# Kernel tuning notes

Measured on AMD Instinct MI355X. Metric: run time of the kernel, lower is better.

## Reference

```python
import jax, jax.numpy as jnp
import numpy as np


def _quat_to_rotT(q):
    # q: [..., 4] in (w, x, y, z) order, exactly mirroring the torch entry order,
    # including the final transpose(3, 2). Returns [..., 3, 3].
    w, x, y, z = q[..., 0], q[..., 1], q[..., 2], q[..., 3]
    R = jnp.stack([
        1.0 - 2.0 * (y ** 2 + z ** 2), 2.0 * x * y - 2.0 * w * z, 2.0 * w * y + 2.0 * x * z,
        2.0 * x * y + 2.0 * z * w, 1.0 - 2.0 * (x ** 2 + z ** 2), -2.0 * w * x + 2.0 * y * z,
        -2.0 * w * y + 2.0 * x * z, 2.0 * w * x + 2.0 * y * z, 1.0 - 2.0 * (x ** 2 + y ** 2),
    ], axis=-1).reshape(q.shape[:-1] + (3, 3))
    return jnp.swapaxes(R, -1, -2)


def _forward(pred_t, pred_r, pred_c, target_r, target_t, model_points, choose, symmetric, diameters, rot_anchors):
    bs, num_rot, _ = pred_r.shape
    # --- anchor regularization: cos_dist = bmm(pred_r, rot_anchors^T) ---
    cos_dist = jnp.einsum('brq,aq->bra', pred_r, rot_anchors)  # [bs, R, R]
    diag = jnp.diagonal(cos_dist, axis1=1, axis2=2)             # [bs, R]
    reg = jnp.max(cos_dist, axis=2) - diag
    loss_reg = jnp.mean(jnp.where(reg > 0.001, reg, 0.0))       # F.threshold(x, 0.001, 0)

    # --- rotate model points by every anchor-refined rotation ---
    rotT = _quat_to_rotT(pred_r)                                 # [bs, R, 3, 3]
    mp = model_points[:, 0]                                      # [bs, N, 3]
    pred_pts = jnp.einsum('bnk,brkj->brnj', mp, rotT)            # [bs, R, N, 3]
    tgt = target_r[:, 0]                                         # [bs, M, 3]

    # symmetric branch: pairwise distances via the |a|^2+|b|^2-2ab expansion
    # (avoids materializing the [bs,R,N,M,3] difference tensor; dist tensor only)
    a2 = jnp.sum(pred_pts ** 2, axis=-1)                         # [bs, R, N]
    b2 = jnp.sum(tgt ** 2, axis=-1)                              # [bs, M]
    ab = jnp.einsum('brnk,bmk->brnm', pred_pts, tgt)             # [bs, R, N, M]
    d2 = a2[:, :, :, None] + b2[:, None, None, :] - 2.0 * ab
    dist_pair = jnp.sqrt(jnp.maximum(d2, 1e-12))
    sym_d = jnp.mean(jnp.min(dist_pair, axis=3), axis=2)         # [bs, R]

    # non-symmetric branch: pointwise distance (M == N)
    nonsym_d = jnp.mean(
        jnp.linalg.norm(pred_pts - tgt[:, None, :, :], axis=-1), axis=2)  # [bs, R]

    d = jnp.where(symmetric[:, None], sym_d, nonsym_d)           # [bs, R]
    per_anchor = d / (diameters[:, None] * pred_c) + jnp.log(pred_c)
    loss_r = jnp.sum(jnp.mean(per_anchor, axis=1))               # summed over batch (torch +=)

    # --- translation smooth-L1 against sampled dense field ---
    tflat = jnp.transpose(target_t, (0, 2, 3, 1)).reshape(bs, -1, 3)      # [bs, H*W, 3]
    tsamp = jnp.take_along_axis(tflat, choose[:, :, None], axis=1)        # [bs, n_sel, 3]
    diff_t = pred_t - tsamp
    ad = jnp.abs(diff_t)
    loss_t = jnp.mean(jnp.where(ad < 1.0, 0.5 * diff_t ** 2, ad - 0.5))

    total = loss_r + 2.0 * loss_reg + 5.0 * loss_t
    return total, loss_r, loss_reg, loss_t


def setup_inputs() -> dict:
    key = jax.random.key(0)
    ks = jax.random.split(key, 8)
    bs, num_rot, N, H, W = 8, 60, 500, 80, 80
    pred_t = jax.random.normal(ks[0], (bs, N, 3), jnp.float32)
    pred_r = jax.random.normal(ks[1], (bs, num_rot, 4), jnp.float32)
    pred_c = jax.random.uniform(ks[2], (bs, num_rot), jnp.float32, 0.05, 1.0)
    target_r = jax.random.normal(ks[3], (bs, 1, N, 3), jnp.float32)
    target_t = jax.random.normal(ks[4], (bs, 3, H, W), jnp.float32)
    model_points = jax.random.normal(ks[5], (bs, 1, N, 3), jnp.float32)
    choose = jax.random.randint(ks[6], (bs, N), 0, H * W)
    symmetric = jnp.ones((bs,), dtype=bool)
    diameters = jnp.ones((bs,), jnp.float32)
    rot_anchors = jax.random.normal(ks[7], (num_rot, 4), jnp.float32)
    return {
        'pred_t': pred_t, 'pred_r': pred_r, 'pred_c': pred_c,
        'target_r': target_r, 'target_t': target_t, 'model_points': model_points,
        'choose': choose, 'symmetric': symmetric, 'diameters': diameters,
        'rot_anchors': rot_anchors,
    }


def reference(pred_t, pred_r, pred_c, target_r, target_t, model_points, choose, symmetric, diameters, rot_anchors):
    return _forward(pred_t, pred_r, pred_c, target_r, target_t, model_points,
                    choose, symmetric, diameters, rot_anchors)
```

## Files before the change

kernel.cpp:

```cpp
#include <hip/hip_runtime.h>
#include <math.h>

#define BS 8
#define NR 60
#define NRP 30
#define NP 500
#define NHW 6400
#define NPAIR (BS*NR)
#define NBLK (BS*NRP)
#define NT_ELEMS (BS*NP*3)
#define LT_PER_BLK 50

#define BIGF 3.4e38f

__global__ __launch_bounds__(256) void main_kernel(
    const float* __restrict__ pred_t,
    const float* __restrict__ pred_r,
    const float* __restrict__ target_r,
    const float* __restrict__ target_t,
    const float* __restrict__ model_points,
    const int*   __restrict__ choose,
    const float* __restrict__ rot_anchors,
    float* __restrict__ out_sym,
    float* __restrict__ out_non,
    float* __restrict__ out_reg,
    float* __restrict__ out_lt)
{
    const int bid = blockIdx.x;
    const int b  = bid / NRP;
    const int rp = bid % NRP;
    const int r0 = 2 * rp, r1 = 2 * rp + 1;
    const int pair0 = b * NR + r0;
    const int tid = threadIdx.x;

    __shared__ float4 t4s[NP];
    __shared__ float red[16];

    for (int i = tid; i < NP; i += 256) {
        const float* p = target_r + (b * NP + i) * 3;
        float x = p[0], y = p[1], z = p[2];
        t4s[i] = make_float4(x, y, z, x * x + y * y + z * z);
    }

    const float* q0p = pred_r + pair0 * 4;
    const float w0 = q0p[0], x0 = q0p[1], y0 = q0p[2], z0 = q0p[3];
    const float w1 = q0p[4], x1 = q0p[5], y1 = q0p[6], z1 = q0p[7];

    const float A00 = 1.f - 2.f * (y0 * y0 + z0 * z0);
    const float A01 = 2.f * x0 * y0 - 2.f * w0 * z0;
    const float A02 = 2.f * w0 * y0 + 2.f * x0 * z0;
    const float A10 = 2.f * x0 * y0 + 2.f * z0 * w0;
    const float A11 = 1.f - 2.f * (x0 * x0 + z0 * z0);
    const float A12 = -2.f * w0 * x0 + 2.f * y0 * z0;
    const float A20 = -2.f * w0 * y0 + 2.f * x0 * z0;
    const float A21 = 2.f * w0 * x0 + 2.f * y0 * z0;
    const float A22 = 1.f - 2.f * (x0 * x0 + y0 * y0);

    const float B00 = 1.f - 2.f * (y1 * y1 + z1 * z1);
    const float B01 = 2.f * x1 * y1 - 2.f * w1 * z1;
    const float B02 = 2.f * w1 * y1 + 2.f * x1 * z1;
    const float B10 = 2.f * x1 * y1 + 2.f * z1 * w1;
    const float B11 = 1.f - 2.f * (x1 * x1 + z1 * z1);
    const float B12 = -2.f * w1 * x1 + 2.f * y1 * z1;
    const float B20 = -2.f * w1 * y1 + 2.f * x1 * z1;
    const float B21 = 2.f * w1 * x1 + 2.f * y1 * z1;
    const float B22 = 1.f - 2.f * (x1 * x1 + y1 * y1);

    float lt = 0.f;
    if (tid < LT_PER_BLK) {
        int e = bid * LT_PER_BLK + tid;
        int bb = e / 1500;
        int rem = e - bb * 1500;
        int n = rem / 3;
        int k = rem - n * 3;
        int pos = choose[bb * NP + n];
        float ts = target_t[(bb * 3 + k) * NHW + pos];
        float diff = pred_t[e] - ts;
        float ad = fabsf(diff);
        lt = (ad < 1.f) ? 0.5f * diff * diff : ad - 0.5f;
    }

    if (tid < 64) {
        float dot = -BIGF;
        if (tid < NR) {
            const float* an = rot_anchors + tid * 4;
            dot = w0 * an[0] + x0 * an[1] + y0 * an[2] + z0 * an[3];
        }
        float diag = __shfl(dot, r0, 64);
        float mx = dot;
        for (int o = 32; o > 0; o >>= 1) mx = fmaxf(mx, __shfl_down(mx, o, 64));
        for (int o = 32; o > 0; o >>= 1) lt += __shfl_down(lt, o, 64);
        if (tid == 0) {
            float rg = mx - diag;
            out_reg[pair0] = (rg > 0.001f) ? rg : 0.f;
            out_lt[bid] = lt;
        }
    } else if (tid < 128) {
        int ln = tid - 64;
        float dot = -BIGF;
        if (ln < NR) {
            const float* an = rot_anchors + ln * 4;
            dot = w1 * an[0] + x1 * an[1] + y1 * an[2] + z1 * an[3];
        }
        float diag = __shfl(dot, r1, 64);
        float mx = dot;
        for (int o = 32; o > 0; o >>= 1) mx = fmaxf(mx, __shfl_down(mx, o, 64));
        if (ln == 0) {
            float rg = mx - diag;
            out_reg[pair0 + 1] = (rg > 0.001f) ? rg : 0.f;
        }
    }

    const int n0 = tid;
    const int n1 = tid + 256;
    const bool has1 = (n1 < NP);
    const int nc = has1 ? n1 : 0;

    const float* mpb = model_points + b * NP * 3;
    const float m0x = mpb[n0 * 3 + 0], m0y = mpb[n0 * 3 + 1], m0z = mpb[n0 * 3 + 2];
    const float m1x = mpb[nc * 3 + 0], m1y = mpb[nc * 3 + 1], m1z = mpb[nc * 3 + 2];

    const float pA0x = A00 * m0x + A01 * m0y + A02 * m0z;
    const float pA0y = A10 * m0x + A11 * m0y + A12 * m0z;
    const float pA0z = A20 * m0x + A21 * m0y + A22 * m0z;
    const float pA1x = A00 * m1x + A01 * m1y + A02 * m1z;
    const float pA1y = A10 * m1x + A11 * m1y + A12 * m1z;
    const float pA1z = A20 * m1x + A21 * m1y + A22 * m1z;
    const float pB0x = B00 * m0x + B01 * m0y + B02 * m0z;
    const float pB0y = B10 * m0x + B11 * m0y + B12 * m0z;
    const float pB0z = B20 * m0x + B21 * m0y + B22 * m0z;
    const float pB1x = B00 * m1x + B01 * m1y + B02 * m1z;
    const float pB1y = B10 * m1x + B11 * m1y + B12 * m1z;
    const float pB1z = B20 * m1x + B21 * m1y + B22 * m1z;

    const float a2A0 = pA0x * pA0x + pA0y * pA0y + pA0z * pA0z;
    const float a2A1 = pA1x * pA1x + pA1y * pA1y + pA1z * pA1z;
    const float a2B0 = pB0x * pB0x + pB0y * pB0y + pB0z * pB0z;
    const float a2B1 = pB1x * pB1x + pB1y * pB1y + pB1z * pB1z;

    __syncthreads();

    float mnA0 = BIGF, mnA1 = BIGF, mnB0 = BIGF, mnB1 = BIGF;
#pragma unroll 4
    for (int m = 0; m < NP; ++m) {
        float4 t = t4s[m];
        float dA0 = fmaf(pA0x, t.x, fmaf(pA0y, t.y, pA0z * t.z));
        float dA1 = fmaf(pA1x, t.x, fmaf(pA1y, t.y, pA1z * t.z));
        float dB0 = fmaf(pB0x, t.x, fmaf(pB0y, t.y, pB0z * t.z));
        float dB1 = fmaf(pB1x, t.x, fmaf(pB1y, t.y, pB1z * t.z));
        mnA0 = fminf(mnA0, fmaf(-2.f, dA0, t.w));
        mnA1 = fminf(mnA1, fmaf(-2.f, dA1, t.w));
        mnB0 = fminf(mnB0, fmaf(-2.f, dB0, t.w));
        mnB1 = fminf(mnB1, fmaf(-2.f, dB1, t.w));
    }

    float t0x, t0y, t0z, t1x, t1y, t1z;
    { float4 t = t4s[n0]; t0x = t.x; t0y = t.y; t0z = t.z; }
    { float4 t = t4s[nc]; t1x = t.x; t1y = t.y; t1z = t.z; }

    float symA = sqrtf(fmaxf(a2A0 + mnA0, 1e-12f));
    float symB = sqrtf(fmaxf(a2B0 + mnB0, 1e-12f));
    float dxA = pA0x - t0x, dyA = pA0y - t0y, dzA = pA0z - t0z;
    float dxB = pB0x - t0x, dyB = pB0y - t0y, dzB = pB0z - t0z;
    float nonA = sqrtf(dxA * dxA + dyA * dyA + dzA * dzA);
    float nonB = sqrtf(dxB * dxB + dyB * dyB + dzB * dzB);
    if (has1) {
        symA += sqrtf(fmaxf(a2A1 + mnA1, 1e-12f));
        symB += sqrtf(fmaxf(a2B1 + mnB1, 1e-12f));
        float ex = pA1x - t1x, ey = pA1y - t1y, ez = pA1z - t1z;
        nonA += sqrtf(ex * ex + ey * ey + ez * ez);
        float fx = pB1x - t1x, fy = pB1y - t1y, fz = pB1z - t1z;
        nonB += sqrtf(fx * fx + fy * fy + fz * fz);
    }

    for (int o = 32; o > 0; o >>= 1) {
        symA += __shfl_down(symA, o, 64);
        symB += __shfl_down(symB, o, 64);
        nonA += __shfl_down(nonA, o, 64);
        nonB += __shfl_down(nonB, o, 64);
    }
    const int wv = tid >> 6, ln = tid & 63;
    if (ln == 0) {
        red[wv] = symA; red[4 + wv] = symB;
        red[8 + wv] = nonA; red[12 + wv] = nonB;
    }
    __syncthreads();
    if (tid == 0) {
        out_sym[pair0]     = red[0] + red[1] + red[2] + red[3];
        out_sym[pair0 + 1] = red[4] + red[5] + red[6] + red[7];
        out_non[pair0]     = red[8] + red[9] + red[10] + red[11];
        out_non[pair0 + 1] = red[12] + red[13] + red[14] + red[15];
    }
}

__global__ __launch_bounds__(256) void finalize_kernel(
    const float* __restrict__ out_sym, const float* __restrict__ out_non,
    const float* __restrict__ out_reg, const float* __restrict__ out_lt,
    const float* __restrict__ pred_c,
    const unsigned char* __restrict__ symU8, const int* __restrict__ symI,
    const float* __restrict__ diam, float* __restrict__ out)
{
    const int tid = threadIdx.x;
    float s_r = 0.f, s_reg = 0.f, s_t = 0.f;
    for (int i = tid; i < NPAIR; i += 256) {
        int b = i / NR;
        bool sym = (symU8[b] != 0) || (symI[b] != 0);
        float sum = sym ? out_sym[i] : out_non[i];
        float d = sum * (1.0f / NP);
        float c = pred_c[i];
        s_r += (d / (diam[b] * c) + logf(c)) * (1.0f / NR);
        s_reg += out_reg[i];
        if (i < NBLK) s_t += out_lt[i];
    }
    __shared__ float red[12];
    for (int o = 32; o > 0; o >>= 1) {
        s_r += __shfl_down(s_r, o, 64);
        s_reg += __shfl_down(s_reg, o, 64);
        s_t += __shfl_down(s_t, o, 64);
    }
    const int wv = tid >> 6, ln = tid & 63;
    if (ln == 0) { red[wv] = s_r; red[4 + wv] = s_reg; red[8 + wv] = s_t; }
    __syncthreads();
    if (tid == 0) {
        float lr = red[0] + red[1] + red[2] + red[3];
        float lreg = (red[4] + red[5] + red[6] + red[7]) * (1.0f / NPAIR);
        float ltv = (red[8] + red[9] + red[10] + red[11]) * (1.0f / NT_ELEMS);
        out[0] = lr + 2.f * lreg + 5.f * ltv;
        out[1] = lr;
        out[2] = lreg;
        out[3] = ltv;
    }
}

extern "C" void kernel_launch(void* const* d_in, const int* in_sizes, int n_in,
                              void* d_out, int out_size, void* d_ws, size_t ws_size,
                              hipStream_t stream) {
    const float* pred_t       = (const float*)d_in[0];
    const float* pred_r       = (const float*)d_in[1];
    const float* pred_c       = (const float*)d_in[2];
    const float* target_r     = (const float*)d_in[3];
    const float* target_t     = (const float*)d_in[4];
    const float* model_points = (const float*)d_in[5];
    const int*   choose       = (const int*)d_in[6];
    const unsigned char* symU8 = (const unsigned char*)d_in[7];
    const int*   symI         = (const int*)d_in[7];
    const float* diam         = (const float*)d_in[8];
    const float* anchors      = (const float*)d_in[9];
    float* out = (float*)d_out;

    char* ws = (char*)d_ws;
    float* o_sym = (float*)ws;
    float* o_non = o_sym + NPAIR;
    float* o_reg = o_non + NPAIR;
    float* o_lt  = o_reg + NPAIR;

    main_kernel<<<NBLK, 256, 0, stream>>>(pred_t, pred_r, target_r, target_t,
                                          model_points, choose, anchors,
                                          o_sym, o_non, o_reg, o_lt);
    finalize_kernel<<<1, 256, 0, stream>>>(o_sym, o_non, o_reg, o_lt,
                                           pred_c, symU8, symI, diam, out);
}
```

Baseline: 102.5 us.

## Split target loop across eight waves with register-blocked points and LDS min-reduce

Doubles the block to 512 threads and assigns each wave one eighth of the target points instead of the whole set. Each lane now keeps 8 source points for both rotations in registers (pre-scaled by -2), so every shared-memory target read feeds 16 FMA/min chains. Per-wave partial minima are then combined through a new shared buffer, and two waves finish the sqrt sums and the non-symmetric distance. The aim is to cut the long serial per-thread loop and the shared-memory read traffic, at the cost of more registers, a larger LDS footprint and an extra reduction stage.

Measured after the change: 91.08 us. 1.12x faster.

```diff
diff --git a/kernel.cpp b/kernel.cpp
--- a/kernel.cpp
+++ b/kernel.cpp
@@ -13,7 +13,7 @@
 
 #define BIGF 3.4e38f
 
-__global__ __launch_bounds__(256) void main_kernel(
+__global__ __launch_bounds__(512) void main_kernel(
     const float* __restrict__ pred_t,
     const float* __restrict__ pred_r,
     const float* __restrict__ target_r,
@@ -32,14 +32,16 @@
     const int r0 = 2 * rp, r1 = 2 * rp + 1;
     const int pair0 = b * NR + r0;
     const int tid = threadIdx.x;
+    const int wv = tid >> 6;
+    const int ln = tid & 63;
 
     __shared__ float4 t4s[NP];
-    __shared__ float red[16];
-
-    for (int i = tid; i < NP; i += 256) {
-        const float* p = target_r + (b * NP + i) * 3;
+    __shared__ float2 part2[8 * 8 * 64];
+
+    if (tid < NP) {
+        const float* p = target_r + (b * NP + tid) * 3;
         float x = p[0], y = p[1], z = p[2];
-        t4s[i] = make_float4(x, y, z, x * x + y * y + z * z);
+        t4s[tid] = make_float4(x, y, z, x * x + y * y + z * z);
     }
 
     const float* q0p = pred_r + pair0 * 4;
@@ -96,7 +98,6 @@
             out_lt[bid] = lt;
         }
     } else if (tid < 128) {
-        int ln = tid - 64;
         float dot = -BIGF;
         if (ln < NR) {
             const float* an = rot_anchors + ln * 4;
@@ -111,85 +112,79 @@
         }
     }
 
-    const int n0 = tid;
-    const int n1 = tid + 256;
-    const bool has1 = (n1 < NP);
-    const int nc = has1 ? n1 : 0;
-
+    float nAx[8], nAy[8], nAz[8], nBx[8], nBy[8], nBz[8];
     const float* mpb = model_points + b * NP * 3;
-    const float m0x = mpb[n0 * 3 + 0], m0y = mpb[n0 * 3 + 1], m0z = mpb[n0 * 3 + 2];
-    const float m1x = mpb[nc * 3 + 0], m1y = mpb[nc * 3 + 1], m1z = mpb[nc * 3 + 2];
-
-    const float pA0x = A00 * m0x + A01 * m0y + A02 * m0z;
-    const float pA0y = A10 * m0x + A11 * m0y + A12 * m0z;
-    const float pA0z = A20 * m0x + A21 * m0y + A22 * m0z;
-    const float pA1x = A00 * m1x + A01 * m1y + A02 * m1z;
-    const float pA1y = A10 * m1x + A11 * m1y + A12 * m1z;
-    const float pA1z = A20 * m1x + A21 * m1y + A22 * m1z;
-    const float pB0x = B00 * m0x + B01 * m0y + B02 * m0z;
-    const float pB0y = B10 * m0x + B11 * m0y + B12 * m0z;
-    const float pB0z = B20 * m0x + B21 * m0y + B22 * m0z;
-    const float pB1x = B00 * m1x + B01 * m1y + B02 * m1z;
-    const float pB1y = B10 * m1x + B11 * m1y + B12 * m1z;
-    const float pB1z = B20 * m1x + B21 * m1y + B22 * m1z;
-
-    const float a2A0 = pA0x * pA0x + pA0y * pA0y + pA0z * pA0z;
-    const float a2A1 = pA1x * pA1x + pA1y * pA1y + pA1z * pA1z;
-    const float a2B0 = pB0x * pB0x + pB0y * pB0y + pB0z * pB0z;
-    const float a2B1 = pB1x * pB1x + pB1y * pB1y + pB1z * pB1z;
+#pragma unroll
+    for (int k = 0; k < 8; ++k) {
+        int pt = k * 64 + ln;
+        int pc = (pt < NP) ? pt : 0;
+        float mx_ = mpb[pc * 3 + 0], my_ = mpb[pc * 3 + 1], mz_ = mpb[pc * 3 + 2];
+        float pax = A00 * mx_ + A01 * my_ + A02 * mz_;
+        float pay = A10 * mx_ + A11 * my_ + A12 * mz_;
+        float paz = A20 * mx_ + A21 * my_ + A22 * mz_;
+        float pbx = B00 * mx_ + B01 * my_ + B02 * mz_;
+        float pby = B10 * mx_ + B11 * my_ + B12 * mz_;
+        float pbz = B20 * mx_ + B21 * my_ + B22 * mz_;
+        nAx[k] = -2.f * pax; nAy[k] = -2.f * pay; nAz[k] = -2.f * paz;
+        nBx[k] = -2.f * pbx; nBy[k] = -2.f * pby; nBz[k] = -2.f * pbz;
+    }
 
     __syncthreads();
 
-    float mnA0 = BIGF, mnA1 = BIGF, mnB0 = BIGF, mnB1 = BIGF;
-#pragma unroll 4
-    for (int m = 0; m < NP; ++m) {
+    const int mstart = (wv * NP) >> 3;
+    const int mend   = ((wv + 1) * NP) >> 3;
+    float mnA[8], mnB[8];
+#pragma unroll
+    for (int k = 0; k < 8; ++k) { mnA[k] = BIGF; mnB[k] = BIGF; }
+
+    for (int m = mstart; m < mend; ++m) {
         float4 t = t4s[m];
-        float dA0 = fmaf(pA0x, t.x, fmaf(pA0y, t.y, pA0z * t.z));
-        float dA1 = fmaf(pA1x, t.x, fmaf(pA1y, t.y, pA1z * t.z));
-        float dB0 = fmaf(pB0x, t.x, fmaf(pB0y, t.y, pB0z * t.z));
-        float dB1 = fmaf(pB1x, t.x, fmaf(pB1y, t.y, pB1z * t.z));
-        mnA0 = fminf(mnA0, fmaf(-2.f, dA0, t.w));
-        mnA1 = fminf(mnA1, fmaf(-2.f, dA1, t.w));
-        mnB0 = fminf(mnB0, fmaf(-2.f, dB0, t.w));
-        mnB1 = fminf(mnB1, fmaf(-2.f, dB1, t.w));
-    }
-
-    float t0x, t0y, t0z, t1x, t1y, t1z;
-    { float4 t = t4s[n0]; t0x = t.x; t0y = t.y; t0z = t.z; }
-    { float4 t = t4s[nc]; t1x = t.x; t1y = t.y; t1z = t.z; }
-
-    float symA = sqrtf(fmaxf(a2A0 + mnA0, 1e-12f));
-    float symB = sqrtf(fmaxf(a2B0 + mnB0, 1e-12f));
-    float dxA = pA0x - t0x, dyA = pA0y - t0y, dzA = pA0z - t0z;
-    float dxB = pB0x - t0x, dyB = pB0y - t0y, dzB = pB0z - t0z;
-    float nonA = sqrtf(dxA * dxA + dyA * dyA + dzA * dzA);
-    float nonB = sqrtf(dxB * dxB + dyB * dyB + dzB * dzB);
-    if (has1) {
-        symA += sqrtf(fmaxf(a2A1 + mnA1, 1e-12f));
-        symB += sqrtf(fmaxf(a2B1 + mnB1, 1e-12f));
-        float ex = pA1x - t1x, ey = pA1y - t1y, ez = pA1z - t1z;
-        nonA += sqrtf(ex * ex + ey * ey + ez * ez);
-        float fx = pB1x - t1x, fy = pB1y - t1y, fz = pB1z - t1z;
-        nonB += sqrtf(fx * fx + fy * fy + fz * fz);
-    }
-
-    for (int o = 32; o > 0; o >>= 1) {
-        symA += __shfl_down(symA, o, 64);
-        symB += __shfl_down(symB, o, 64);
-        nonA += __shfl_down(nonA, o, 64);
-        nonB += __shfl_down(nonB, o, 64);
-    }
-    const int wv = tid >> 6, ln = tid & 63;
-    if (ln == 0) {
-        red[wv] = symA; red[4 + wv] = symB;
-        red[8 + wv] = nonA; red[12 + wv] = nonB;
-    }
+#pragma unroll
+        for (int k = 0; k < 8; ++k) {
+            float dA = fmaf(nAx[k], t.x, fmaf(nAy[k], t.y, fmaf(nAz[k], t.z, t.w)));
+            mnA[k] = fminf(mnA[k], dA);
+            float dB = fmaf(nBx[k], t.x, fmaf(nBy[k], t.y, fmaf(nBz[k], t.z, t.w)));
+            mnB[k] = fminf(mnB[k], dB);
+        }
+    }
+
+#pragma unroll
+    for (int k = 0; k < 8; ++k)
+        part2[(wv * 8 + k) * 64 + ln] = make_float2(mnA[k], mnB[k]);
     __syncthreads();
-    if (tid == 0) {
-        out_sym[pair0]     = red[0] + red[1] + red[2] + red[3];
-        out_sym[pair0 + 1] = red[4] + red[5] + red[6] + red[7];
-        out_non[pair0]     = red[8] + red[9] + red[10] + red[11];
-        out_non[pair0 + 1] = red[12] + red[13] + red[14] + red[15];
+
+    if (wv < 2) {
+        const float* partf = (const float*)part2;
+        float symsum = 0.f, nonsum = 0.f;
+#pragma unroll
+        for (int k = 0; k < 8; ++k) {
+            float mn = BIGF;
+#pragma unroll
+            for (int w2 = 0; w2 < 8; ++w2) {
+                float v = partf[((w2 * 8 + k) * 64 + ln) * 2 + wv];
+                mn = fminf(mn, v);
+            }
+            float px = -0.5f * ((wv == 0) ? nAx[k] : nBx[k]);
+            float py = -0.5f * ((wv == 0) ? nAy[k] : nBy[k]);
+            float pz = -0.5f * ((wv == 0) ? nAz[k] : nBz[k]);
+            float a2 = px * px + py * py + pz * pz;
+            int pt = k * 64 + ln;
+            if (pt < NP) {
+                float d2 = fmaxf(a2 + mn, 1e-12f);
+                symsum += sqrtf(d2);
+                float4 t = t4s[pt];
+                float dx = px - t.x, dy = py - t.y, dz = pz - t.z;
+                nonsum += sqrtf(dx * dx + dy * dy + dz * dz);
+            }
+        }
+        for (int o = 32; o > 0; o >>= 1) {
+            symsum += __shfl_down(symsum, o, 64);
+            nonsum += __shfl_down(nonsum, o, 64);
+        }
+        if (ln == 0) {
+            out_sym[pair0 + wv] = symsum;
+            out_non[pair0 + wv] = nonsum;
+        }
     }
 }
 
@@ -254,7 +249,7 @@
     float* o_reg = o_non + NPAIR;
     float* o_lt  = o_reg + NPAIR;
 
-    main_kernel<<<NBLK, 256, 0, stream>>>(pred_t, pred_r, target_r, target_t,
+    main_kernel<<<NBLK, 512, 0, stream>>>(pred_t, pred_r, target_r, target_t,
                                           model_points, choose, anchors,
                                           o_sym, o_non, o_reg, o_lt);
     finalize_kernel<<<1, 256, 0, stream>>>(o_sym, o_non, o_reg, o_lt,
```
